# Performance work log

Hardware: AMD Instinct MI355X
Metric: run time of the kernel (lower is better)

The kernel has to match this reference:

```python
import jax, jax.numpy as jnp
import numpy as np

EPS = 1e-6
B, I, N, Wd, R = 128, 512, 512, 32, 4


def setup_inputs() -> dict:
    key = jax.random.key(0)
    ks = jax.random.split(key, 32)
    inp = {
        "xi": jax.random.normal(ks[0], (B, I), jnp.float32),
        "memory": jax.random.normal(ks[1], (B, N, Wd), jnp.float32),
        "link_matrix": jax.random.uniform(ks[2], (B, N, N), jnp.float32),
        "precedence": jax.random.uniform(ks[3], (B, N), jnp.float32),
        "read_weights": jax.random.uniform(ks[4], (B, R, N), jnp.float32),
        "write_weights": jax.random.uniform(ks[5], (B, N), jnp.float32),
        "usage": jax.random.uniform(ks[6], (B, N), jnp.float32),
    }
    # 10 independent linear heads (weight [out, in], bias [out]) as in independent_linears=True
    dims = [("rk", R * Wd), ("rs", R), ("wk", Wd), ("ws", 1), ("ev", Wd),
            ("wv", Wd), ("fg", R), ("ag", 1), ("wg", 1), ("rm", 3 * R)]
    scale = 1.0 / np.sqrt(I).astype(np.float32)
    for i, (nm, d) in enumerate(dims):
        inp["W_" + nm] = jax.random.normal(ks[7 + 2 * i], (d, I), jnp.float32) * scale
        inp["b_" + nm] = jax.random.normal(ks[8 + 2 * i], (d,), jnp.float32) * 0.01
    return inp


def reference(xi, memory, link_matrix, precedence, read_weights, write_weights, usage,
              W_rk, b_rk, W_rs, b_rs, W_wk, b_wk, W_ws, b_ws, W_ev, b_ev,
              W_wv, b_wv, W_fg, b_fg, W_ag, b_ag, W_wg, b_wg, W_rm, b_rm):
    b, n, w = memory.shape
    r = b_rs.shape[0]
    lin = lambda Wm, bm: xi @ Wm.T + bm

    # interface vectors
    read_keys = jnp.tanh(lin(W_rk, b_rk)).reshape(b, r, w)          # [B,R,W]
    read_str = jax.nn.softplus(lin(W_rs, b_rs))                      # [B,R]
    write_key = jnp.tanh(lin(W_wk, b_wk))                            # [B,W]
    write_str = jax.nn.softplus(lin(W_ws, b_ws))                     # [B,1]
    erase = jax.nn.sigmoid(lin(W_ev, b_ev))                          # [B,W]
    write_vec = jnp.tanh(lin(W_wv, b_wv))                            # [B,W]
    free = jax.nn.sigmoid(lin(W_fg, b_fg))                           # [B,R]
    alloc_g = jax.nn.sigmoid(lin(W_ag, b_ag))                        # [B,1]
    write_g = jax.nn.sigmoid(lin(W_wg, b_wg))                        # [B,1]
    modes = jax.nn.softmax(lin(W_rm, b_rm).reshape(b, r, 3), axis=2)

    # usage update (memory retention)
    psi = jnp.prod(1.0 - free[:, :, None] * read_weights, axis=1)    # [B,N]
    usage = (usage + write_weights - usage * write_weights) * psi

    # allocation weighting via sorted usage
    idx = jnp.argsort(usage, axis=1)
    su = jnp.take_along_axis(usage, idx, axis=1)
    prod_excl = jnp.concatenate(
        [jnp.ones((b, 1), su.dtype), jnp.cumprod(su, axis=1)[:, :-1]], axis=1)
    alloc_sorted = (1.0 - su) * prod_excl
    alloc = jnp.zeros_like(usage).at[jnp.arange(b)[:, None], idx].set(alloc_sorted)

    # write content addressing (cosine similarity)
    mem_norm = jnp.linalg.norm(memory, axis=2)                       # [B,N]
    wsim = jnp.einsum('bnw,bw->bn', memory, write_key) / (
        mem_norm * jnp.linalg.norm(write_key, axis=1, keepdims=True) + EPS)
    wc = jax.nn.softmax(write_str * wsim, axis=1)                    # [B,N]

    ww = write_g * (alloc_g * alloc + (1.0 - alloc_g) * wc)          # [B,N]

    # memory write (erase then add)
    memory = memory * (1.0 - ww[:, :, None] * erase[:, None, :]) \
             + ww[:, :, None] * write_vec[:, None, :]

    # temporal link matrix + precedence update
    link = (1.0 - ww[:, :, None] - ww[:, None, :]) * link_matrix \
           + ww[:, :, None] * precedence[:, None, :]
    link = link * (1.0 - jnp.eye(n, dtype=link.dtype))
    precedence = (1.0 - jnp.sum(ww, axis=1, keepdims=True)) * precedence + ww

    # directional read weights from previous read weights
    fw = jnp.einsum('bnm,brm->brn', link, read_weights)              # forward: L w
    bw = jnp.einsum('bmn,brm->brn', link, read_weights)              # backward: L^T w

    # read content addressing on updated memory
    mem_norm2 = jnp.linalg.norm(memory, axis=2)
    rsim = jnp.einsum('bnw,brw->brn', memory, read_keys) / (
        mem_norm2[:, None, :] * jnp.linalg.norm(read_keys, axis=2, keepdims=True) + EPS)
    rc = jax.nn.softmax(read_str[:, :, None] * rsim, axis=2)         # [B,R,N]

    read_weights = modes[:, :, 0:1] * bw + modes[:, :, 1:2] * rc + modes[:, :, 2:3] * fw
    read_vectors = jnp.einsum('brn,bnw->brw', read_weights, memory)  # [B,R,W]
    return read_vectors, memory, link, precedence, read_weights, ww, usage
```

## Files before the change

### kernel.cpp

```cpp
#include <hip/hip_runtime.h>
#include <math.h>

#define BB 128
#define ID 512
#define NN 512
#define WDIM 32
#define RR 4
#define EPSF 1e-6f
#define NTILE 16

#define OFF_RV   ((size_t)0)
#define OFF_MEM  (OFF_RV + (size_t)BB*RR*WDIM)
#define OFF_LINK (OFF_MEM + (size_t)BB*NN*WDIM)
#define OFF_PREC (OFF_LINK + (size_t)BB*NN*NN)
#define OFF_RW   (OFF_PREC + (size_t)BB*NN)
#define OFF_WW   (OFF_RW + (size_t)BB*RR*NN)
#define OFF_USG  (OFF_WW + (size_t)BB*NN)

#define IF_RK 0
#define IF_RS 128
#define IF_WK 132
#define IF_WS 164
#define IF_EV 165
#define IF_WV 197
#define IF_FG 229
#define IF_AG 233
#define IF_WG 234
#define IF_RM 235

#define WS_IFACE ((size_t)0)
#define WS_FW    (WS_IFACE + (size_t)BB*256)
#define WS_BW    (WS_FW + (size_t)BB*RR*NN)
#define WS_PART  WS_BW
#define WS_PART_FLOATS ((size_t)BB*NTILE*RR*NN)

__device__ __forceinline__ float sigm(float x) { return 1.0f / (1.0f + expf(-x)); }
__device__ __forceinline__ float softplusf(float x) { return fmaxf(x, 0.0f) + log1pf(expf(-fabsf(x))); }

struct HeadArgs {
  const float *Wrk, *brk, *Wrs, *brs, *Wwk, *bwk, *Wws, *bws, *Wev, *bev,
              *Wwv, *bwv, *Wfg, *bfg, *Wag, *bag, *Wwg, *bwg, *Wrm, *brm;
};

__global__ __launch_bounds__(256) void k1_heads(const float* __restrict__ xi, HeadArgs ha,
                                                float* __restrict__ iface) {
  __shared__ __align__(16) float xs[ID];
  __shared__ float raw[256];
  int b = blockIdx.x, t = threadIdx.x;
  for (int i = t; i < ID; i += 256) xs[i] = xi[b * ID + i];
  __syncthreads();
  const float* Ws[10] = {ha.Wrk, ha.Wrs, ha.Wwk, ha.Wws, ha.Wev, ha.Wwv, ha.Wfg, ha.Wag, ha.Wwg, ha.Wrm};
  const float* bs[10] = {ha.brk, ha.brs, ha.bwk, ha.bws, ha.bev, ha.bwv, ha.bfg, ha.bag, ha.bwg, ha.brm};
  const int off[11] = {0, 128, 132, 164, 165, 197, 229, 233, 234, 235, 247};
  float val = 0.0f;
  int h = -1, row = 0;
  if (t < 247) {
    for (int k = 0; k < 10; ++k)
      if (t >= off[k] && t < off[k + 1]) { h = k; row = t - off[k]; }
    const float4* w4 = (const float4*)(Ws[h] + row * ID);
    const float4* x4 = (const float4*)xs;
    float acc = 0.0f;
    for (int i = 0; i < ID / 4; ++i) {
      float4 w = w4[i], x = x4[i];
      acc += w.x * x.x + w.y * x.y + w.z * x.z + w.w * x.w;
    }
    val = acc + bs[h][row];
  }
  raw[t] = val;
  __syncthreads();
  if (t < 247) {
    float o;
    if (h == 0 || h == 2 || h == 5) o = tanhf(val);
    else if (h == 1 || h == 3) o = softplusf(val);
    else if (h == 9) {
      int g = (t - 235) / 3;
      float a0 = raw[235 + g * 3], a1 = raw[236 + g * 3], a2 = raw[237 + g * 3];
      float mx = fmaxf(a0, fmaxf(a1, a2));
      o = expf(val - mx) / (expf(a0 - mx) + expf(a1 - mx) + expf(a2 - mx));
    } else o = sigm(val);
    iface[b * 256 + t] = o;
  }
}

__global__ __launch_bounds__(512) void k2_write(const float* __restrict__ mem_in,
                                                const float* __restrict__ prec_in,
                                                const float* __restrict__ rw_in,
                                                const float* __restrict__ wwt_in,
                                                const float* __restrict__ usg_in,
                                                const float* __restrict__ iface,
                                                float* __restrict__ bw,
                                                float* __restrict__ out) {
  __shared__ __align__(16) float sif[256];
  __shared__ float sv[NN];
  __shared__ int si[NN];
  __shared__ float salloc[NN];
  __shared__ float sred[8];
  __shared__ float swt[8];
  int b = blockIdx.x, tid = threadIdx.x;
  int lane = tid & 63, wave = tid >> 6;

  for (int i = tid; i < RR * NN; i += 512) bw[(size_t)b * RR * NN + i] = 0.0f;

  if (tid < 256) sif[tid] = iface[b * 256 + tid];
  __syncthreads();

  const float* rwb = rw_in + (size_t)b * RR * NN;
  float psi = 1.0f;
#pragma unroll
  for (int r = 0; r < RR; r++) psi *= 1.0f - sif[IF_FG + r] * rwb[r * NN + tid];
  float u = usg_in[b * NN + tid], wwt = wwt_in[b * NN + tid];
  u = (u + wwt - u * wwt) * psi;

  float v = u; int idx = tid;
  for (int k = 2; k <= NN; k <<= 1) {
    for (int j = k >> 1; j > 0; j >>= 1) {
      int p = tid ^ j;
      float pv; int pi;
      if (j >= 64) {
        sv[tid] = v; si[tid] = idx;
        __syncthreads();
        pv = sv[p]; pi = si[p];
        __syncthreads();
      } else {
        pv = __shfl_xor(v, j);
        pi = __shfl_xor(idx, j);
      }
      bool mineSmaller = (v < pv) || (v == pv && idx < pi);
      bool keepMin = (((tid & k) == 0) == (tid < p));
      bool take = keepMin ? !mineSmaller : mineSmaller;
      if (take) { v = pv; idx = pi; }
    }
  }

  float pr = v;
#pragma unroll
  for (int o = 1; o < 64; o <<= 1) {
    float q = __shfl_up(pr, o);
    if (lane >= o) pr *= q;
  }
  if (lane == 63) swt[wave] = pr;
  __syncthreads();
  float wp = 1.0f;
#pragma unroll
  for (int w = 0; w < 8; w++) if (w < wave) wp *= swt[w];
  float ep = __shfl_up(pr, 1);
  if (lane == 0) ep = 1.0f;
  float alloc_sorted = (1.0f - v) * (wp * ep);
  salloc[idx] = alloc_sorted;
  __syncthreads();
  float alloc = salloc[tid];

  const float4* mrow = (const float4*)(mem_in + ((size_t)b * NN + tid) * WDIM);
  float4 mv[8];
  float dot = 0, nrm = 0, wkn = 0;
#pragma unroll
  for (int i = 0; i < 8; i++) {
    float4 m = mrow[i];
    mv[i] = m;
    const float4 kk = *(const float4*)&sif[IF_WK + 4 * i];
    dot += m.x * kk.x + m.y * kk.y + m.z * kk.z + m.w * kk.w;
    nrm += m.x * m.x + m.y * m.y + m.z * m.z + m.w * m.w;
    wkn += kk.x * kk.x + kk.y * kk.y + kk.z * kk.z + kk.w * kk.w;
  }
  float s = sif[IF_WS] * (dot / (sqrtf(nrm) * sqrtf(wkn) + EPSF));

  float m8 = s;
#pragma unroll
  for (int d = 32; d > 0; d >>= 1) m8 = fmaxf(m8, __shfl_down(m8, d));
  if (lane == 0) sred[wave] = m8;
  __syncthreads();
  float mx = sred[0];
#pragma unroll
  for (int w = 1; w < 8; w++) mx = fmaxf(mx, sred[w]);
  __syncthreads();
  float e = expf(s - mx);
  float sm = e;
#pragma unroll
  for (int d = 32; d > 0; d >>= 1) sm += __shfl_down(sm, d);
  if (lane == 0) sred[wave] = sm;
  __syncthreads();
  float esum = 0;
#pragma unroll
  for (int w = 0; w < 8; w++) esum += sred[w];
  __syncthreads();
  float wc = e / esum;

  float ww = sif[IF_WG] * (sif[IF_AG] * alloc + (1.0f - sif[IF_AG]) * wc);
  out[OFF_WW + b * NN + tid] = ww;
  out[OFF_USG + b * NN + tid] = u;

  float ws_ = ww;
#pragma unroll
  for (int d = 32; d > 0; d >>= 1) ws_ += __shfl_down(ws_, d);
  if (lane == 0) sred[wave] = ws_;
  __syncthreads();
  float wsum = 0;
#pragma unroll
  for (int w = 0; w < 8; w++) wsum += sred[w];
  out[OFF_PREC + b * NN + tid] = (1.0f - wsum) * prec_in[b * NN + tid] + ww;

  float* mo = out + OFF_MEM + ((size_t)b * NN + tid) * WDIM;
#pragma unroll
  for (int i = 0; i < 8; i++) {
    float4 m = mv[i];
    float4 o;
    o.x = m.x * (1.0f - ww * sif[IF_EV + 4 * i + 0]) + ww * sif[IF_WV + 4 * i + 0];
    o.y = m.y * (1.0f - ww * sif[IF_EV + 4 * i + 1]) + ww * sif[IF_WV + 4 * i + 1];
    o.z = m.z * (1.0f - ww * sif[IF_EV + 4 * i + 2]) + ww * sif[IF_WV + 4 * i + 2];
    o.w = m.w * (1.0f - ww * sif[IF_EV + 4 * i + 3]) + ww * sif[IF_WV + 4 * i + 3];
    ((float4*)mo)[i] = o;
  }
}

template<int PARTIAL>
__global__ __launch_bounds__(256) void k3_link(const float* __restrict__ link_in,
                                               const float* __restrict__ prec_in,
                                               const float* __restrict__ rw_in,
                                               const float* __restrict__ ww_out,
                                               float* __restrict__ link_out,
                                               float* __restrict__ fw,
                                               float* __restrict__ bw) {
  __shared__ __align__(16) float sww[NN];
  __shared__ __align__(16) float sprec[NN];
  __shared__ __align__(16) float srw[RR * NN];
  __shared__ float sbw[RR * NN];
  __shared__ float sfw[RR * 32];
  int b = blockIdx.y, tile = blockIdx.x, tid = threadIdx.x;
  for (int i = tid; i < NN; i += 256) {
    sww[i] = ww_out[b * NN + i];
    sprec[i] = prec_in[b * NN + i];
  }
  for (int i = tid; i < RR * NN; i += 256) {
    srw[i] = rw_in[(size_t)b * RR * NN + i];
    sbw[i] = 0.0f;
  }
  __syncthreads();

  int wave = tid >> 6, lane = tid & 63;
  float4 cww[2], cpr[2], crw[RR][2];
#pragma unroll
  for (int h = 0; h < 2; h++) {
    cww[h] = ((const float4*)sww)[h * 64 + lane];
    cpr[h] = ((const float4*)sprec)[h * 64 + lane];
#pragma unroll
    for (int r = 0; r < RR; r++) crw[r][h] = ((const float4*)(srw + r * NN))[h * 64 + lane];
  }

  float bwa[RR][8];
#pragma unroll
  for (int r = 0; r < RR; r++)
#pragma unroll
    for (int j = 0; j < 8; j++) bwa[r][j] = 0.0f;

  const size_t lbase = (size_t)b * NN * NN;
  const float* lbp = link_in + lbase;
  int row0 = tile * 32 + wave;

  float4 nv0 = ((const float4*)(lbp + (size_t)row0 * NN))[lane];
  float4 nv1 = ((const float4*)(lbp + (size_t)row0 * NN))[64 + lane];

  for (int i = 0; i < 8; i++) {
    int row = row0 + 4 * i;
    float4 cv[2] = {nv0, nv1};
    if (i < 7) {
      const float4* Ln = (const float4*)(lbp + (size_t)(row + 4) * NN);
      nv0 = Ln[lane];
      nv1 = Ln[64 + lane];
    }
    float wwr = sww[row];
    float rwr[RR] = {srw[row], srw[NN + row], srw[2 * NN + row], srw[3 * NN + row]};
    float4* Lo = (float4*)(link_out + lbase + (size_t)row * NN);
    float fp[RR] = {0, 0, 0, 0};
#pragma unroll
    for (int h = 0; h < 2; h++) {
      float4 lv = cv[h];
      float l[4] = {lv.x, lv.y, lv.z, lv.w};
      float wc[4] = {cww[h].x, cww[h].y, cww[h].z, cww[h].w};
      float pc[4] = {cpr[h].x, cpr[h].y, cpr[h].z, cpr[h].w};
      int c0 = h * 256 + 4 * lane;
#pragma unroll
      for (int j = 0; j < 4; j++) {
        float ln = (1.0f - wwr - wc[j]) * l[j] + wwr * pc[j];
        if (c0 + j == row) ln = 0.0f;
        l[j] = ln;
#pragma unroll
        for (int r = 0; r < RR; r++) bwa[r][h * 4 + j] += ln * rwr[r];
      }
#pragma unroll
      for (int r = 0; r < RR; r++) {
        float rc0 = (r == 0) ? crw[0][h].x : (r == 1) ? crw[1][h].x : (r == 2) ? crw[2][h].x : crw[3][h].x;
        float rc1 = (r == 0) ? crw[0][h].y : (r == 1) ? crw[1][h].y : (r == 2) ? crw[2][h].y : crw[3][h].y;
        float rc2 = (r == 0) ? crw[0][h].z : (r == 1) ? crw[1][h].z : (r == 2) ? crw[2][h].z : crw[3][h].z;
        float rc3 = (r == 0) ? crw[0][h].w : (r == 1) ? crw[1][h].w : (r == 2) ? crw[2][h].w : crw[3][h].w;
        fp[r] += l[0] * rc0 + l[1] * rc1 + l[2] * rc2 + l[3] * rc3;
      }
      float4 ov = {l[0], l[1], l[2], l[3]};
      Lo[h * 64 + lane] = ov;
    }
#pragma unroll
    for (int d = 32; d > 0; d >>= 1) {
      fp[0] += __shfl_down(fp[0], d);
      fp[1] += __shfl_down(fp[1], d);
      fp[2] += __shfl_down(fp[2], d);
      fp[3] += __shfl_down(fp[3], d);
    }
    if (lane == 0) {
      int rl = wave + 4 * i;
      sfw[0 * 32 + rl] = fp[0];
      sfw[1 * 32 + rl] = fp[1];
      sfw[2 * 32 + rl] = fp[2];
      sfw[3 * 32 + rl] = fp[3];
    }
  }
  __syncthreads();

  if (tid < RR * 32) {
    int r = tid >> 5, j = tid & 31;
    fw[(size_t)b * RR * NN + r * NN + tile * 32 + j] = sfw[tid];
  }

  for (int w = 0; w < 4; w++) {
    if (wave == w) {
#pragma unroll
      for (int r = 0; r < RR; r++)
#pragma unroll
        for (int h = 0; h < 2; h++)
#pragma unroll
          for (int j = 0; j < 4; j++)
            sbw[r * NN + h * 256 + 4 * lane + j] += bwa[r][h * 4 + j];
    }
    __syncthreads();
  }
  if (PARTIAL) {
    float* bp = bw + ((size_t)(b * NTILE + tile)) * RR * NN;
    for (int i = tid; i < RR * NN; i += 256) bp[i] = sbw[i];
  } else {
    float* bp = bw + (size_t)b * RR * NN;
    for (int i = tid; i < RR * NN; i += 256) atomicAdd(&bp[i], sbw[i]);
  }
}

template<int PARTIAL>
__global__ __launch_bounds__(512) void k4_read(const float* __restrict__ iface,
                                               const float* __restrict__ fw,
                                               const float* __restrict__ bw,
                                               float* __restrict__ out) {
  __shared__ __align__(16) float srk[WDIM];
  __shared__ float sred[8];
  __shared__ float srwn[NN];
  __shared__ float spart[16][WDIM];
  int b = blockIdx.x >> 2, r = blockIdx.x & 3;
  int tid = threadIdx.x, lane = tid & 63, wave = tid >> 6;
  const float* ifb = iface + b * 256;
  if (tid < WDIM) srk[tid] = ifb[IF_RK + r * WDIM + tid];
  __syncthreads();
  float rkn2 = 0;
#pragma unroll
  for (int w = 0; w < WDIM; w++) { float v = srk[w]; rkn2 += v * v; }
  float rkn = sqrtf(rkn2);

  const float* mem = out + OFF_MEM + (size_t)b * NN * WDIM;
  const float4* mrow = (const float4*)(mem + (size_t)tid * WDIM);
  float d = 0, nrm = 0;
#pragma unroll
  for (int i = 0; i < 8; i++) {
    float4 m = mrow[i];
    const float4 kk = *(const float4*)&srk[4 * i];
    nrm += m.x * m.x + m.y * m.y + m.z * m.z + m.w * m.w;
    d += m.x * kk.x + m.y * kk.y + m.z * kk.z + m.w * kk.w;
  }
  float s = ifb[IF_RS + r] * (d / (sqrtf(nrm) * rkn + EPSF));

  float m8 = s;
#pragma unroll
  for (int dd = 32; dd > 0; dd >>= 1) m8 = fmaxf(m8, __shfl_down(m8, dd));
  if (lane == 0) sred[wave] = m8;
  __syncthreads();
  float mx = sred[0];
#pragma unroll
  for (int w = 1; w < 8; w++) mx = fmaxf(mx, sred[w]);
  __syncthreads();
  float e = expf(s - mx);
  float sm = e;
#pragma unroll
  for (int dd = 32; dd > 0; dd >>= 1) sm += __shfl_down(sm, dd);
  if (lane == 0) sred[wave] = sm;
  __syncthreads();
  float esum = 0;
#pragma unroll
  for (int w = 0; w < 8; w++) esum += sred[w];
  float rc = e / esum;

  float bwv;
  if (PARTIAL) {
    const float* pp = bw + ((size_t)b * NTILE * RR + r) * NN + tid;
    float acc = 0.0f;
#pragma unroll
    for (int t = 0; t < NTILE; t++) acc += pp[(size_t)t * RR * NN];
    bwv = acc;
  } else {
    bwv = bw[((size_t)b * RR + r) * NN + tid];
  }
  float fwv = fw[((size_t)b * RR + r) * NN + tid];
  float m0 = ifb[IF_RM + 3 * r], m1 = ifb[IF_RM + 3 * r + 1], m2 = ifb[IF_RM + 3 * r + 2];
  float v = m0 * bwv + m1 * rc + m2 * fwv;
  srwn[tid] = v;
  out[OFF_RW + ((size_t)b * RR + r) * NN + tid] = v;
  __syncthreads();

  int w = tid & 31, part = tid >> 5;
  float acc = 0;
  const float* mp = mem + (size_t)part * 32 * WDIM + w;
  const float* rp = srwn + part * 32;
#pragma unroll
  for (int n = 0; n < 32; n++) acc += rp[n] * mp[(size_t)n * WDIM];
  spart[part][w] = acc;
  __syncthreads();
  if (tid < WDIM) {
    float vv = 0;
#pragma unroll
    for (int p = 0; p < 16; p++) vv += spart[p][tid];
    out[OFF_RV + ((size_t)b * RR + r) * WDIM + tid] = vv;
  }
}

extern "C" void kernel_launch(void* const* d_in, const int* in_sizes, int n_in,
                              void* d_out, int out_size, void* d_ws, size_t ws_size,
                              hipStream_t stream) {
  const float* xi = (const float*)d_in[0];
  const float* mem = (const float*)d_in[1];
  const float* link = (const float*)d_in[2];
  const float* prec = (const float*)d_in[3];
  const float* rw = (const float*)d_in[4];
  const float* wwt = (const float*)d_in[5];
  const float* usg = (const float*)d_in[6];
  HeadArgs ha;
  ha.Wrk = (const float*)d_in[7];  ha.brk = (const float*)d_in[8];
  ha.Wrs = (const float*)d_in[9];  ha.brs = (const float*)d_in[10];
  ha.Wwk = (const float*)d_in[11]; ha.bwk = (const float*)d_in[12];
  ha.Wws = (const float*)d_in[13]; ha.bws = (const float*)d_in[14];
  ha.Wev = (const float*)d_in[15]; ha.bev = (const float*)d_in[16];
  ha.Wwv = (const float*)d_in[17]; ha.bwv = (const float*)d_in[18];
  ha.Wfg = (const float*)d_in[19]; ha.bfg = (const float*)d_in[20];
  ha.Wag = (const float*)d_in[21]; ha.bag = (const float*)d_in[22];
  ha.Wwg = (const float*)d_in[23]; ha.bwg = (const float*)d_in[24];
  ha.Wrm = (const float*)d_in[25]; ha.brm = (const float*)d_in[26];

  float* out = (float*)d_out;
  float* ws = (float*)d_ws;
  float* iface = ws + WS_IFACE;
  float* fwbuf = ws + WS_FW;
  float* bwbuf = ws + WS_BW;

  const size_t need_part_bytes = (WS_PART + WS_PART_FLOATS) * sizeof(float);
  const bool use_partial = ws_size >= need_part_bytes;

  k1_heads<<<BB, 256, 0, stream>>>(xi, ha, iface);
  k2_write<<<BB, 512, 0, stream>>>(mem, prec, rw, wwt, usg, iface, bwbuf, out);
  if (use_partial) {
    k3_link<1><<<dim3(NTILE, BB), 256, 0, stream>>>(link, prec, rw, out + OFF_WW, out + OFF_LINK, fwbuf, ws + WS_PART);
    k4_read<1><<<BB * RR, 512, 0, stream>>>(iface, fwbuf, ws + WS_PART, out);
  } else {
    k3_link<0><<<dim3(NTILE, BB), 256, 0, stream>>>(link, prec, rw, out + OFF_WW, out + OFF_LINK, fwbuf, bwbuf);
    k4_read<0><<<BB * RR, 512, 0, stream>>>(iface, fwbuf, bwbuf, out);
  }
}
```

Measured before the change: 352.6 us.

## Replace bitonic sort with rank product, nontemporal link stores, fuse read heads

The allocation weighting no longer uses a bitonic sort plus prefix product. Each thread now multiplies together every usage value that ranks below its own, an O(N) loop over shared memory with no barriers inside it. Link matrix outputs are written with nontemporal stores to avoid polluting cache, and forward weights are written directly instead of staged through shared memory. The read kernel now handles all four read heads per block, reusing each memory row load across heads, which cuts the block count by four but adds register pressure.

```diff
diff --git a/kernel.cpp b/kernel.cpp
--- a/kernel.cpp
+++ b/kernel.cpp
@@ -8,6 +8,8 @@
 #define RR 4
 #define EPSF 1e-6f
 #define NTILE 16
+
+typedef float nt_float4 __attribute__((ext_vector_type(4)));
 
 #define OFF_RV   ((size_t)0)
 #define OFF_MEM  (OFF_RV + (size_t)BB*RR*WDIM)
@@ -91,11 +93,8 @@
                                                 float* __restrict__ bw,
                                                 float* __restrict__ out) {
   __shared__ __align__(16) float sif[256];
-  __shared__ float sv[NN];
-  __shared__ int si[NN];
-  __shared__ float salloc[NN];
+  __shared__ __align__(16) float su[NN];
   __shared__ float sred[8];
-  __shared__ float swt[8];
   int b = blockIdx.x, tid = threadIdx.x;
   int lane = tid & 63, wave = tid >> 6;
 
@@ -111,44 +110,19 @@
   float u = usg_in[b * NN + tid], wwt = wwt_in[b * NN + tid];
   u = (u + wwt - u * wwt) * psi;
 
-  float v = u; int idx = tid;
-  for (int k = 2; k <= NN; k <<= 1) {
-    for (int j = k >> 1; j > 0; j >>= 1) {
-      int p = tid ^ j;
-      float pv; int pi;
-      if (j >= 64) {
-        sv[tid] = v; si[tid] = idx;
-        __syncthreads();
-        pv = sv[p]; pi = si[p];
-        __syncthreads();
-      } else {
-        pv = __shfl_xor(v, j);
-        pi = __shfl_xor(idx, j);
-      }
-      bool mineSmaller = (v < pv) || (v == pv && idx < pi);
-      bool keepMin = (((tid & k) == 0) == (tid < p));
-      bool take = keepMin ? !mineSmaller : mineSmaller;
-      if (take) { v = pv; idx = pi; }
-    }
-  }
-
-  float pr = v;
-#pragma unroll
-  for (int o = 1; o < 64; o <<= 1) {
-    float q = __shfl_up(pr, o);
-    if (lane >= o) pr *= q;
-  }
-  if (lane == 63) swt[wave] = pr;
-  __syncthreads();
-  float wp = 1.0f;
-#pragma unroll
-  for (int w = 0; w < 8; w++) if (w < wave) wp *= swt[w];
-  float ep = __shfl_up(pr, 1);
-  if (lane == 0) ep = 1.0f;
-  float alloc_sorted = (1.0f - v) * (wp * ep);
-  salloc[idx] = alloc_sorted;
-  __syncthreads();
-  float alloc = salloc[tid];
+  su[tid] = u;
+  __syncthreads();
+
+  float pr = 1.0f;
+#pragma unroll 4
+  for (int j = 0; j < NN; j += 4) {
+    float4 uu = *(const float4*)&su[j];
+    pr *= ((uu.x < u) || (uu.x == u && (j + 0) < tid)) ? uu.x : 1.0f;
+    pr *= ((uu.y < u) || (uu.y == u && (j + 1) < tid)) ? uu.y : 1.0f;
+    pr *= ((uu.z < u) || (uu.z == u && (j + 2) < tid)) ? uu.z : 1.0f;
+    pr *= ((uu.w < u) || (uu.w == u && (j + 3) < tid)) ? uu.w : 1.0f;
+  }
+  float alloc = (1.0f - u) * pr;
 
   const float4* mrow = (const float4*)(mem_in + ((size_t)b * NN + tid) * WDIM);
   float4 mv[8];
@@ -224,7 +198,6 @@
   __shared__ __align__(16) float sprec[NN];
   __shared__ __align__(16) float srw[RR * NN];
   __shared__ float sbw[RR * NN];
-  __shared__ float sfw[RR * 32];
   int b = blockIdx.y, tile = blockIdx.x, tid = threadIdx.x;
   for (int i = tid; i < NN; i += 256) {
     sww[i] = ww_out[b * NN + i];
@@ -269,7 +242,7 @@
     }
     float wwr = sww[row];
     float rwr[RR] = {srw[row], srw[NN + row], srw[2 * NN + row], srw[3 * NN + row]};
-    float4* Lo = (float4*)(link_out + lbase + (size_t)row * NN);
+    nt_float4* Lo = (nt_float4*)(link_out + lbase + (size_t)row * NN);
     float fp[RR] = {0, 0, 0, 0};
 #pragma unroll
     for (int h = 0; h < 2; h++) {
@@ -294,8 +267,8 @@
         float rc3 = (r == 0) ? crw[0][h].w : (r == 1) ? crw[1][h].w : (r == 2) ? crw[2][h].w : crw[3][h].w;
         fp[r] += l[0] * rc0 + l[1] * rc1 + l[2] * rc2 + l[3] * rc3;
       }
-      float4 ov = {l[0], l[1], l[2], l[3]};
-      Lo[h * 64 + lane] = ov;
+      nt_float4 ov = {l[0], l[1], l[2], l[3]};
+      __builtin_nontemporal_store(ov, &Lo[h * 64 + lane]);
     }
 #pragma unroll
     for (int d = 32; d > 0; d >>= 1) {
@@ -305,18 +278,12 @@
       fp[3] += __shfl_down(fp[3], d);
     }
     if (lane == 0) {
-      int rl = wave + 4 * i;
-      sfw[0 * 32 + rl] = fp[0];
-      sfw[1 * 32 + rl] = fp[1];
-      sfw[2 * 32 + rl] = fp[2];
-      sfw[3 * 32 + rl] = fp[3];
-    }
-  }
-  __syncthreads();
-
-  if (tid < RR * 32) {
-    int r = tid >> 5, j = tid & 31;
-    fw[(size_t)b * RR * NN + r * NN + tile * 32 + j] = sfw[tid];
+      float* fwb = fw + (size_t)b * RR * NN;
+      fwb[0 * NN + row] = fp[0];
+      fwb[1 * NN + row] = fp[1];
+      fwb[2 * NN + row] = fp[2];
+      fwb[3 * NN + row] = fp[3];
+    }
   }
 
   for (int w = 0; w < 4; w++) {
@@ -345,82 +312,117 @@
                                                const float* __restrict__ fw,
                                                const float* __restrict__ bw,
                                                float* __restrict__ out) {
-  __shared__ __align__(16) float srk[WDIM];
-  __shared__ float sred[8];
-  __shared__ float srwn[NN];
-  __shared__ float spart[16][WDIM];
-  int b = blockIdx.x >> 2, r = blockIdx.x & 3;
+  __shared__ __align__(16) float srk[RR][WDIM];
+  __shared__ float smax[8][RR];
+  __shared__ float ssum[8][RR];
+  __shared__ __align__(16) float srwn[RR][NN];
+  __shared__ float spart[RR][16][WDIM];
+  int b = blockIdx.x;
   int tid = threadIdx.x, lane = tid & 63, wave = tid >> 6;
   const float* ifb = iface + b * 256;
-  if (tid < WDIM) srk[tid] = ifb[IF_RK + r * WDIM + tid];
-  __syncthreads();
-  float rkn2 = 0;
-#pragma unroll
-  for (int w = 0; w < WDIM; w++) { float v = srk[w]; rkn2 += v * v; }
-  float rkn = sqrtf(rkn2);
+  if (tid < RR * WDIM) srk[tid >> 5][tid & 31] = ifb[IF_RK + tid];
+  __syncthreads();
+
+  float rkn[RR];
+#pragma unroll
+  for (int r = 0; r < RR; r++) {
+    float a = 0;
+#pragma unroll
+    for (int w = 0; w < WDIM; w++) { float t = srk[r][w]; a += t * t; }
+    rkn[r] = sqrtf(a);
+  }
 
   const float* mem = out + OFF_MEM + (size_t)b * NN * WDIM;
   const float4* mrow = (const float4*)(mem + (size_t)tid * WDIM);
-  float d = 0, nrm = 0;
+  float d[RR] = {0, 0, 0, 0};
+  float nrm = 0;
 #pragma unroll
   for (int i = 0; i < 8; i++) {
     float4 m = mrow[i];
-    const float4 kk = *(const float4*)&srk[4 * i];
     nrm += m.x * m.x + m.y * m.y + m.z * m.z + m.w * m.w;
-    d += m.x * kk.x + m.y * kk.y + m.z * kk.z + m.w * kk.w;
-  }
-  float s = ifb[IF_RS + r] * (d / (sqrtf(nrm) * rkn + EPSF));
-
-  float m8 = s;
-#pragma unroll
-  for (int dd = 32; dd > 0; dd >>= 1) m8 = fmaxf(m8, __shfl_down(m8, dd));
-  if (lane == 0) sred[wave] = m8;
-  __syncthreads();
-  float mx = sred[0];
-#pragma unroll
-  for (int w = 1; w < 8; w++) mx = fmaxf(mx, sred[w]);
-  __syncthreads();
-  float e = expf(s - mx);
-  float sm = e;
-#pragma unroll
-  for (int dd = 32; dd > 0; dd >>= 1) sm += __shfl_down(sm, dd);
-  if (lane == 0) sred[wave] = sm;
-  __syncthreads();
-  float esum = 0;
-#pragma unroll
-  for (int w = 0; w < 8; w++) esum += sred[w];
-  float rc = e / esum;
-
-  float bwv;
-  if (PARTIAL) {
-    const float* pp = bw + ((size_t)b * NTILE * RR + r) * NN + tid;
-    float acc = 0.0f;
-#pragma unroll
-    for (int t = 0; t < NTILE; t++) acc += pp[(size_t)t * RR * NN];
-    bwv = acc;
-  } else {
-    bwv = bw[((size_t)b * RR + r) * NN + tid];
-  }
-  float fwv = fw[((size_t)b * RR + r) * NN + tid];
-  float m0 = ifb[IF_RM + 3 * r], m1 = ifb[IF_RM + 3 * r + 1], m2 = ifb[IF_RM + 3 * r + 2];
-  float v = m0 * bwv + m1 * rc + m2 * fwv;
-  srwn[tid] = v;
-  out[OFF_RW + ((size_t)b * RR + r) * NN + tid] = v;
+#pragma unroll
+    for (int r = 0; r < RR; r++) {
+      const float4 kk = *(const float4*)&srk[r][4 * i];
+      d[r] += m.x * kk.x + m.y * kk.y + m.z * kk.z + m.w * kk.w;
+    }
+  }
+  float sq = sqrtf(nrm);
+  float s[RR];
+#pragma unroll
+  for (int r = 0; r < RR; r++) s[r] = ifb[IF_RS + r] * (d[r] / (sq * rkn[r] + EPSF));
+
+  float m8[RR] = {s[0], s[1], s[2], s[3]};
+#pragma unroll
+  for (int dd = 32; dd > 0; dd >>= 1)
+#pragma unroll
+    for (int r = 0; r < RR; r++) m8[r] = fmaxf(m8[r], __shfl_down(m8[r], dd));
+  if (lane == 0)
+#pragma unroll
+    for (int r = 0; r < RR; r++) smax[wave][r] = m8[r];
+  __syncthreads();
+  float e[RR], sm[RR];
+#pragma unroll
+  for (int r = 0; r < RR; r++) {
+    float mx = smax[0][r];
+#pragma unroll
+    for (int w = 1; w < 8; w++) mx = fmaxf(mx, smax[w][r]);
+    e[r] = expf(s[r] - mx);
+    sm[r] = e[r];
+  }
+#pragma unroll
+  for (int dd = 32; dd > 0; dd >>= 1)
+#pragma unroll
+    for (int r = 0; r < RR; r++) sm[r] += __shfl_down(sm[r], dd);
+  if (lane == 0)
+#pragma unroll
+    for (int r = 0; r < RR; r++) ssum[wave][r] = sm[r];
+  __syncthreads();
+
+  float v[RR];
+#pragma unroll
+  for (int r = 0; r < RR; r++) {
+    float esum = 0;
+#pragma unroll
+    for (int w = 0; w < 8; w++) esum += ssum[w][r];
+    float rc = e[r] / esum;
+
+    float bwv;
+    if (PARTIAL) {
+      float acc = 0.0f;
+#pragma unroll
+      for (int t = 0; t < NTILE; t++)
+        acc += bw[((size_t)(b * NTILE + t)) * RR * NN + r * NN + tid];
+      bwv = acc;
+    } else {
+      bwv = bw[((size_t)b * RR + r) * NN + tid];
+    }
+    float fwv = fw[((size_t)b * RR + r) * NN + tid];
+    float m0 = ifb[IF_RM + 3 * r], m1 = ifb[IF_RM + 3 * r + 1], m2 = ifb[IF_RM + 3 * r + 2];
+    v[r] = m0 * bwv + m1 * rc + m2 * fwv;
+    srwn[r][tid] = v[r];
+    out[OFF_RW + ((size_t)b * RR + r) * NN + tid] = v[r];
+  }
   __syncthreads();
 
   int w = tid & 31, part = tid >> 5;
-  float acc = 0;
+  float acc[RR] = {0, 0, 0, 0};
   const float* mp = mem + (size_t)part * 32 * WDIM + w;
-  const float* rp = srwn + part * 32;
-#pragma unroll
-  for (int n = 0; n < 32; n++) acc += rp[n] * mp[(size_t)n * WDIM];
-  spart[part][w] = acc;
-  __syncthreads();
-  if (tid < WDIM) {
+  const float* rp0 = &srwn[0][part * 32];
+#pragma unroll
+  for (int n = 0; n < 32; n++) {
+    float mvv = mp[(size_t)n * WDIM];
+#pragma unroll
+    for (int r = 0; r < RR; r++) acc[r] += srwn[r][part * 32 + n] * mvv;
+  }
+#pragma unroll
+  for (int r = 0; r < RR; r++) spart[r][part][w] = acc[r];
+  __syncthreads();
+  if (tid < RR * WDIM) {
+    int r = tid >> 5, w2 = tid & 31;
     float vv = 0;
 #pragma unroll
-    for (int p = 0; p < 16; p++) vv += spart[p][tid];
-    out[OFF_RV + ((size_t)b * RR + r) * WDIM + tid] = vv;
+    for (int p = 0; p < 16; p++) vv += spart[r][p][w2];
+    out[OFF_RV + ((size_t)b * RR + r) * WDIM + w2] = vv;
   }
 }
 
@@ -459,9 +461,9 @@
   k2_write<<<BB, 512, 0, stream>>>(mem, prec, rw, wwt, usg, iface, bwbuf, out);
   if (use_partial) {
     k3_link<1><<<dim3(NTILE, BB), 256, 0, stream>>>(link, prec, rw, out + OFF_WW, out + OFF_LINK, fwbuf, ws + WS_PART);
-    k4_read<1><<<BB * RR, 512, 0, stream>>>(iface, fwbuf, ws + WS_PART, out);
+    k4_read<1><<<BB, 512, 0, stream>>>(iface, fwbuf, ws + WS_PART, out);
   } else {
     k3_link<0><<<dim3(NTILE, BB), 256, 0, stream>>>(link, prec, rw, out + OFF_WW, out + OFF_LINK, fwbuf, bwbuf);
-    k4_read<0><<<BB * RR, 512, 0, stream>>>(iface, fwbuf, bwbuf, out);
+    k4_read<0><<<BB, 512, 0, stream>>>(iface, fwbuf, bwbuf, out);
   }
 }
```

After: 375.7 us. +6.5%, slower.
